# Kernel tuning notes

Measured on AMD Instinct MI355X. Metric: run time of the kernel, lower is better.

## Reference

```python
import jax, jax.numpy as jnp
import numpy as np

N_BITS = 16
BATCH = 4194304  # 2**22 tokens
TABLE_SIZE = 2 ** (N_BITS - 1)  # largest CUMULATIVE/FLIP context is n_bits-1 bits


def setup_inputs() -> dict:
    key = jax.random.key(0)
    k1, k2 = jax.random.split(key)
    # input bit tensor [batch, n_bits], values in {0,1}; index n_bits-1 is bit 0 (LSB)
    bits = jax.random.randint(k1, (BATCH, N_BITS), 0, 2, dtype=jnp.int32)
    # per-bit-position RAM lookup tables, padded to the max address space.
    # Binary contents {0,1}, stored as float32 so the flip/XOR math is expressible.
    tables = (jax.random.uniform(k2, (N_BITS, TABLE_SIZE)) < 0.5).astype(jnp.float32)
    return {"bits": bits, "tables": tables}


def reference(bits, tables):
    """BitLevelMapper forward, CUMULATIVE context + FLIP output mode.

    bits:   [B, n_bits] int32 in {0,1}, array index n_bits-1-k holds bit value k (LSB=k=0)
    tables: [n_bits, 2^(n_bits-1)] float32 in {0,1}; row i is the RAM/LUT for bit_pos i.
    For bit_pos i the context is the lowest i bits (bit0..bit_{i-1});
    address = sum_k context_bit_k * 2^k; flip = table[i, address];
    output bit i = input bit i XOR flip.
    """
    n_bits = bits.shape[1]
    bits_rev = bits[:, ::-1]                      # [B, n] column k = bit value k
    k = jnp.arange(n_bits)
    # W[i, k] = 2^k if k < i else 0  -> addr_i = sum_{k<i} bit_k * 2^k (addr_0 = 0)
    W = jnp.where(k[None, :] < k[:, None], (1 << k)[None, :], 0).astype(jnp.int32)
    addr = bits_rev @ W.T                          # [B, n] int32 RAM addresses per bit_pos
    flip = tables[k[None, :], addr]                # [B, n] gather: tables[i, addr[b, i]]
    x = bits_rev.astype(tables.dtype)
    out_rev = x + flip - 2.0 * x * flip            # XOR expressed arithmetically
    return out_rev[:, ::-1]                        # back to original bit-array layout
```

## Files before the change

### kernel.cpp

```cpp
#include <hip/hip_runtime.h>
#include <hip/hip_bf16.h>


#define PACK_WORDS 2048

typedef float vfloat4 __attribute__((ext_vector_type(4)));

__global__ __launch_bounds__(256) void
pack_tables_kernel(const float* __restrict__ tables, unsigned* __restrict__ packed) {
    int g = blockIdx.x * blockDim.x + threadIdx.x;
    bool val = false;
    if (g < 65535) {
        int i = 31 - __clz(g + 1);
        int a = g - ((1 << i) - 1);
        val = tables[i * 32768 + a] != 0.0f;
    }
    unsigned long long m = __ballot(val);
    if ((threadIdx.x & 63) == 0) {
        packed[(g >> 5)]     = (unsigned)m;
        packed[(g >> 5) + 1] = (unsigned)(m >> 32);
    }
}

__global__ __launch_bounds__(256) void
compress_kernel(const int4* __restrict__ bits4, unsigned short* __restrict__ rowv) {
    int t = blockIdx.x * 256 + threadIdx.x;
    int4 m = bits4[t];
    unsigned nb = (unsigned)((m.x << 3) | (m.y << 2) | (m.z << 1) | m.w);
    unsigned part = nb << (12 - ((t & 3) << 2));
    part |= (unsigned)__shfl_xor((int)part, 1, 64);
    part |= (unsigned)__shfl_xor((int)part, 2, 64);
    if ((t & 3) == 0)
        rowv[t >> 2] = (unsigned short)part;
}

__global__ __launch_bounds__(256) void
expand_kernel(const unsigned short* __restrict__ rowv,
              const unsigned* __restrict__ packed,
              vfloat4* __restrict__ out4) {
    __shared__ unsigned tab[PACK_WORDS];
    {
        const int4* p4 = (const int4*)packed;
        int4* t4 = (int4*)tab;
        t4[threadIdx.x]       = p4[threadIdx.x];
        t4[threadIdx.x + 256] = p4[threadIdx.x + 256];
    }
    __syncthreads();

    const size_t base = (size_t)blockIdx.x * 1024 + threadIdx.x;
    const int q4 = (int)(threadIdx.x & 3) << 2;
    #pragma unroll
    for (int it = 0; it < 4; ++it) {
        size_t t = base + (size_t)it * 256;
        unsigned v = rowv[t >> 2];
        float o[4];
        #pragma unroll
        for (int j = 0; j < 4; ++j) {
            int i = 15 - q4 - j;
            unsigned mask = (1u << i) - 1u;
            unsigned bidx = mask + (v & mask);
            unsigned fl   = tab[bidx >> 5] >> (bidx & 31u);
            o[j] = (float)(((v >> i) ^ fl) & 1u);
        }
        vfloat4 f = {o[0], o[1], o[2], o[3]};
        __builtin_nontemporal_store(f, &out4[t]);
    }
}

extern "C" void kernel_launch(void* const* d_in, const int* in_sizes, int n_in,
                              void* d_out, int out_size, void* d_ws, size_t ws_size,
                              hipStream_t stream) {
    const int*      bits   = (const int*)d_in[0];
    const float*    tables = (const float*)d_in[1];
    float*          out    = (float*)d_out;
    unsigned*       packed = (unsigned*)d_ws;
    unsigned short* rowv   = (unsigned short*)((char*)d_ws + 8192);

    int nrows    = in_sizes[0] / 16;
    int nquarter = nrows * 4;

    pack_tables_kernel<<<65536 / 256, 256, 0, stream>>>(tables, packed);

    compress_kernel<<<nquarter / 256, 256, 0, stream>>>((const int4*)bits, rowv);

    expand_kernel<<<nquarter / 1024, 256, 0, stream>>>(rowv, packed,
                                                       (vfloat4*)out);
}
```

Measured before the change: 428.9 us.

## Move table lookups into compress stage with persistent grid; expand only unpacks bits

The bit-packing and table-lookup XOR now happen together in a grid-stride kernel of 2048 blocks. That kernel packs each row into 16 bits, looks up the flip bits in the shared-memory table, and writes the already-XORed 16-bit row. The expand kernel no longer loads the table into shared memory; it only unpacks bits to floats, and its stores are now plain rather than nontemporal. This removes the table preload from the many small expand blocks and spreads the table load over fewer persistent blocks, at the cost of more shuffles in the compress stage.

```diff
diff --git a/kernel.cpp b/kernel.cpp
--- a/kernel.cpp
+++ b/kernel.cpp
@@ -23,21 +23,9 @@
 }
 
 __global__ __launch_bounds__(256) void
-compress_kernel(const int4* __restrict__ bits4, unsigned short* __restrict__ rowv) {
-    int t = blockIdx.x * 256 + threadIdx.x;
-    int4 m = bits4[t];
-    unsigned nb = (unsigned)((m.x << 3) | (m.y << 2) | (m.z << 1) | m.w);
-    unsigned part = nb << (12 - ((t & 3) << 2));
-    part |= (unsigned)__shfl_xor((int)part, 1, 64);
-    part |= (unsigned)__shfl_xor((int)part, 2, 64);
-    if ((t & 3) == 0)
-        rowv[t >> 2] = (unsigned short)part;
-}
-
-__global__ __launch_bounds__(256) void
-expand_kernel(const unsigned short* __restrict__ rowv,
-              const unsigned* __restrict__ packed,
-              vfloat4* __restrict__ out4) {
+transform_kernel(const int4* __restrict__ bits4,
+                 const unsigned* __restrict__ packed,
+                 unsigned short* __restrict__ rowv, int nquarter) {
     __shared__ unsigned tab[PACK_WORDS];
     {
         const int4* p4 = (const int4*)packed;
@@ -47,23 +35,49 @@
     }
     __syncthreads();
 
+    const int q  = threadIdx.x & 3;
+    const int t0 = blockIdx.x * 256 + threadIdx.x;
+    const int stride = gridDim.x * 256;
+
+    for (int t = t0; t < nquarter; t += stride) {
+        int4 m = bits4[t];
+        unsigned nb = (unsigned)((m.x << 3) | (m.y << 2) | (m.z << 1) | m.w);
+        unsigned v  = nb << (12 - (q << 2));
+        v |= (unsigned)__shfl_xor((int)v, 1, 64);
+        v |= (unsigned)__shfl_xor((int)v, 2, 64);
+
+        unsigned r = 0;
+        #pragma unroll
+        for (int jj = 0; jj < 4; ++jj) {
+            int i = (q << 2) + jj;
+            unsigned mask = (1u << i) - 1u;
+            unsigned bidx = mask + (v & mask);
+            unsigned fl   = tab[bidx >> 5] >> (bidx & 31u);
+            r |= (((v >> i) ^ fl) & 1u) << i;
+        }
+        r |= (unsigned)__shfl_xor((int)r, 1, 64);
+        r |= (unsigned)__shfl_xor((int)r, 2, 64);
+
+        if (q == 0)
+            rowv[t >> 2] = (unsigned short)r;
+    }
+}
+
+__global__ __launch_bounds__(256) void
+expand_kernel(const unsigned short* __restrict__ rowv,
+              vfloat4* __restrict__ out4) {
     const size_t base = (size_t)blockIdx.x * 1024 + threadIdx.x;
     const int q4 = (int)(threadIdx.x & 3) << 2;
     #pragma unroll
     for (int it = 0; it < 4; ++it) {
         size_t t = base + (size_t)it * 256;
         unsigned v = rowv[t >> 2];
-        float o[4];
-        #pragma unroll
-        for (int j = 0; j < 4; ++j) {
-            int i = 15 - q4 - j;
-            unsigned mask = (1u << i) - 1u;
-            unsigned bidx = mask + (v & mask);
-            unsigned fl   = tab[bidx >> 5] >> (bidx & 31u);
-            o[j] = (float)(((v >> i) ^ fl) & 1u);
-        }
-        vfloat4 f = {o[0], o[1], o[2], o[3]};
-        __builtin_nontemporal_store(f, &out4[t]);
+        vfloat4 f;
+        f.x = (float)((v >> (15 - q4)) & 1u);
+        f.y = (float)((v >> (14 - q4)) & 1u);
+        f.z = (float)((v >> (13 - q4)) & 1u);
+        f.w = (float)((v >> (12 - q4)) & 1u);
+        out4[t] = f;
     }
 }
 
@@ -81,8 +95,8 @@
 
     pack_tables_kernel<<<65536 / 256, 256, 0, stream>>>(tables, packed);
 
-    compress_kernel<<<nquarter / 256, 256, 0, stream>>>((const int4*)bits, rowv);
+    transform_kernel<<<2048, 256, 0, stream>>>((const int4*)bits, packed,
+                                               rowv, nquarter);
 
-    expand_kernel<<<nquarter / 1024, 256, 0, stream>>>(rowv, packed,
-                                                       (vfloat4*)out);
+    expand_kernel<<<nquarter / 1024, 256, 0, stream>>>(rowv, (vfloat4*)out);
 }
```

Measured after the change: 445.3 us. +3.8%, slower.
